# Kernel optimization log

Measured on AMD Instinct MI355X. Metric: run time of the kernel, lower is better.

Reference implementation:

```python
import jax, jax.numpy as jnp
import numpy as np

B, N, C, H, W = 256, 50000, 3, 32, 32


def setup_inputs() -> dict:
    key = jax.random.key(0)
    k1, k2, k3 = jax.random.split(key, 3)
    inp = jax.random.normal(k1, (B, C, H, W), dtype=jnp.float32)
    train_data = jax.random.normal(k2, (N, C, H, W), dtype=jnp.float32)
    # per-query noise levels in a realistic diffusion range
    sigma = jax.random.uniform(k3, (B,), dtype=jnp.float32) * 1.5 + 0.5
    return {"input": inp, "sigma": sigma, "train_data": train_data}


def reference(input, sigma, train_data):
    """Karras optimal denoiser:
    D(x, sigma) = sum_i y_i * Gau(x; y_i, sigma^2 I) / sum_i Gau(x; y_i, sigma^2 I).
    The Gaussian normalization constant (sigma*sqrt(2*pi))^D cancels in the ratio,
    so this is exactly softmax over -0.5*||x - y_i||^2 / sigma^2 (same math as the
    per-dim product of densities in the original, computed stably in log space).
    """
    b = input.shape[0]
    x = input.reshape(b, -1)                      # [B, D]
    y = train_data.reshape(train_data.shape[0], -1)  # [N, D]
    x2 = jnp.sum(x * x, axis=1, keepdims=True)    # [B, 1]
    y2 = jnp.sum(y * y, axis=1)                   # [N]
    # pairwise squared distances via GEMM: [B, N]
    sqdist = x2 + y2[None, :] - 2.0 * (x @ y.T)
    logw = -0.5 * sqdist / (sigma[:, None] ** 2)  # [B, N]
    w = jax.nn.softmax(logw, axis=1)              # normalized Gaussian weights
    out = w @ y                                   # [B, D] weighted average
    return out.reshape(input.shape)
```

## Files before the change

kernel.cpp:

```cpp
#include <hip/hip_runtime.h>
#include <hip/hip_bf16.h>
#include <type_traits>

#define BQ   256
#define NTR  50000
#define DD   3072
#define NSP  50048
#define NBLK 391
#define CAP  4096
#define DELTA 18.0f

typedef __fp16 f16;
typedef __fp16 f16x2 __attribute__((ext_vector_type(2)));
typedef __fp16 f16x8 __attribute__((ext_vector_type(8)));
typedef float  f32x4 __attribute__((ext_vector_type(4)));

__global__ __launch_bounds__(256) void kx(const float* __restrict__ x, f16* __restrict__ xp) {
    const int t = blockIdx.x * 256 + threadIdx.x;
    const int g = t >> 8, r = t & 255;
    const f32x4* src = (const f32x4*)(x + (size_t)r * DD + (g << 3));
    f32x4 a = src[0], b = src[1];
    union { f16x2 h2[4]; f16x8 h8; } u;
    u.h2[0] = __builtin_amdgcn_cvt_pkrtz(a[0], a[1]);
    u.h2[1] = __builtin_amdgcn_cvt_pkrtz(a[2], a[3]);
    u.h2[2] = __builtin_amdgcn_cvt_pkrtz(b[0], b[1]);
    u.h2[3] = __builtin_amdgcn_cvt_pkrtz(b[2], b[3]);
    ((f16x8*)xp)[t] = u.h8;
}

__global__ __launch_bounds__(256, 2) void kqk(
    const f16* __restrict__ xp, const float* __restrict__ y,
    float* __restrict__ S, float* __restrict__ pmax) {
    __shared__ char Bs[2][16384];

    const int tid = threadIdx.x;
    const int blk = blockIdx.x;
    const int n0  = blk * 128;

    const int ry   = tid >> 1;
    const int kp   = (tid & 1) << 5;
    const int yrow = n0 + ry;
    const bool yval = yrow < NTR;
    const float* ybase = y + (size_t)yrow * DD + kp;
    const int bsw = (ry & 7) << 4;
    int bo[4];
    #pragma unroll
    for (int j = 0; j < 4; ++j) bo[j] = ry * 128 + (((kp << 1) + (j << 4)) ^ bsw);

    const int w = tid >> 6, l = tid & 63;
    const int l15 = l & 15, lg = l >> 4;

    f32x4 acc[4][8] = {};
    float y2a = 0.f;
    f32x4 p[8];

    auto loady = [&](int ks) {
        if (yval) {
            const f32x4* pp = (const f32x4*)(ybase + (ks << 6));
            #pragma unroll
            for (int j = 0; j < 8; ++j) p[j] = pp[j];
        } else {
            #pragma unroll
            for (int j = 0; j < 8; ++j) p[j] = 0.f;
        }
    };
    auto cvtw = [&](int buf) {
        #pragma unroll
        for (int j = 0; j < 8; ++j)
            y2a += p[j][0]*p[j][0] + p[j][1]*p[j][1] + p[j][2]*p[j][2] + p[j][3]*p[j][3];
        union { f16x2 h2[4]; f16x8 h8; } u[4];
        #pragma unroll
        for (int j = 0; j < 4; ++j) {
            u[j].h2[0] = __builtin_amdgcn_cvt_pkrtz(p[2*j][0],   p[2*j][1]);
            u[j].h2[1] = __builtin_amdgcn_cvt_pkrtz(p[2*j][2],   p[2*j][3]);
            u[j].h2[2] = __builtin_amdgcn_cvt_pkrtz(p[2*j+1][0], p[2*j+1][1]);
            u[j].h2[3] = __builtin_amdgcn_cvt_pkrtz(p[2*j+1][2], p[2*j+1][3]);
            *(f16x8*)(&Bs[buf][bo[j]]) = u[j].h8;
        }
    };

    loady(0);
    cvtw(0);
    asm volatile("s_waitcnt lgkmcnt(0)" ::: "memory");
    __builtin_amdgcn_s_barrier();

    const f16x8* ap = (const f16x8*)xp;
    const int arow = (w << 6) + l15;

    for (int ks = 0; ks < 48; ++ks) {
        const int cur = ks & 1;
        if (ks + 1 < 48) loady(ks + 1);
        #pragma unroll
        for (int kk = 0; kk < 2; ++kk) {
            f16x8 af[4];
            #pragma unroll
            for (int fm = 0; fm < 4; ++fm)
                af[fm] = ap[(size_t)((ks << 3) + (kk << 2) + lg) * 256 + arow + (fm << 4)];
            #pragma unroll
            for (int fnh = 0; fnh < 2; ++fnh) {
                f16x8 bf[4];
                #pragma unroll
                for (int fj = 0; fj < 4; ++fj) {
                    int fn = (fnh << 2) + fj;
                    int r = (fn << 4) + l15;
                    bf[fj] = *(const f16x8*)(&Bs[cur][r * 128 + (((kk << 6) + (lg << 4)) ^ ((r & 7) << 4))]);
                }
                #pragma unroll
                for (int fm = 0; fm < 4; ++fm)
                    #pragma unroll
                    for (int fj = 0; fj < 4; ++fj)
                        acc[fm][(fnh << 2) + fj] =
                            __builtin_amdgcn_mfma_f32_16x16x32_f16(af[fm], bf[fj], acc[fm][(fnh << 2) + fj], 0, 0, 0);
            }
        }
        if (ks + 1 < 48) cvtw(cur ^ 1);
        asm volatile("s_waitcnt lgkmcnt(0)" ::: "memory");
        __builtin_amdgcn_s_barrier();
    }

    float* lys = (float*)&Bs[0][0];
    y2a += __shfl_xor(y2a, 1, 64);
    if ((tid & 1) == 0) lys[ry] = y2a;
    __syncthreads();
    float ly2[8];
    #pragma unroll
    for (int fn = 0; fn < 8; ++fn) ly2[fn] = 0.5f * lys[(fn << 4) + l15];
    #pragma unroll
    for (int fm = 0; fm < 4; ++fm) {
        #pragma unroll
        for (int j = 0; j < 4; ++j) {
            float rm = -3.4e38f;
            #pragma unroll
            for (int fn = 0; fn < 8; ++fn) {
                int col = n0 + (fn << 4) + l15;
                float sc = acc[fm][fn][j] - ly2[fn];
                rm = (col < NTR) ? fmaxf(rm, sc) : rm;
            }
            #pragma unroll
            for (int off = 1; off < 16; off <<= 1) rm = fmaxf(rm, __shfl_xor(rm, off, 64));
            if (l15 == 0)
                pmax[(size_t)((w << 6) + (fm << 4) + (lg << 2) + j) * NBLK + blk] = rm;
        }
    }
    #pragma unroll
    for (int fm = 0; fm < 4; ++fm) {
        int row0 = (w << 6) + (fm << 4) + (lg << 2);
        #pragma unroll
        for (int fn = 0; fn < 8; ++fn) {
            int col = n0 + (fn << 4) + l15;
            float* sp = S + (size_t)row0 * NSP + col;
            sp[0]               = acc[fm][fn][0] - ly2[fn];
            sp[NSP]             = acc[fm][fn][1] - ly2[fn];
            sp[2 * (size_t)NSP] = acc[fm][fn][2] - ly2[fn];
            sp[3 * (size_t)NSP] = acc[fm][fn][3] - ly2[fn];
        }
    }
}

__global__ __launch_bounds__(256) void ksel(
    const float* __restrict__ S, const float* __restrict__ pmax,
    const float* __restrict__ sig, unsigned* __restrict__ cnt,
    unsigned* __restrict__ cand) {
    __shared__ float red[4];
    const int b = blockIdx.x, tid = threadIdx.x;
    const float s2 = sig[b] * sig[b];
    const float* pm = pmax + (size_t)b * NBLK;
    float mx = -3.4e38f;
    for (int i = tid; i < NBLK; i += 256) mx = fmaxf(mx, pm[i]);
    #pragma unroll
    for (int o = 1; o < 64; o <<= 1) mx = fmaxf(mx, __shfl_xor(mx, o, 64));
    if ((tid & 63) == 0) red[tid >> 6] = mx;
    __syncthreads();
    mx = fmaxf(fmaxf(red[0], red[1]), fmaxf(red[2], red[3]));
    const float thr = mx - DELTA * s2;
    const f32x4* rowv = (const f32x4*)(S + (size_t)b * NSP);
    for (int i = tid; i < 12500; i += 256) {
        f32x4 s = rowv[i];
        #pragma unroll
        for (int j = 0; j < 4; ++j) {
            if (s[j] >= thr) {
                unsigned idx = atomicAdd(&cnt[b], 1u);
                if (idx < CAP) cand[(size_t)b * CAP + idx] = (unsigned)(4 * i + j);
            }
        }
    }
}

__global__ __launch_bounds__(512) void kpv(
    const float* __restrict__ x, const float* __restrict__ y,
    const float* __restrict__ sig, const unsigned* __restrict__ cnt,
    const unsigned* __restrict__ cand, float* __restrict__ out) {
    __shared__ float xs[DD];
    __shared__ unsigned ci[CAP];
    __shared__ float om[8], ol[8];
    __shared__ float sumv[DD];
    const int b = blockIdx.x, tid = threadIdx.x;
    const int c = (int)(cnt[b] < (unsigned)CAP ? cnt[b] : (unsigned)CAP);
    const float s2 = sig[b] * sig[b];
    const float isc = -0.5f / s2;
    for (int i = tid; i < DD; i += 512) xs[i] = x[(size_t)b * DD + i];
    for (int i = tid; i < c; i += 512) ci[i] = cand[(size_t)b * CAP + i];
    __syncthreads();
    const int w = tid >> 6, l = tid & 63;
    const f32x4* xr = (const f32x4*)xs;

    f32x4 o[12] = {};
    float m = -3.4e38f, ll = 0.f;
    f32x4 A[12], Bv[12];

    auto LD = [&](f32x4* dst, int i) {
        const f32x4* yr = (const f32x4*)(y + (size_t)ci[i] * DD);
        #pragma unroll
        for (int j = 0; j < 12; ++j) dst[j] = yr[(j << 6) + l];
    };
    auto PROC = [&](f32x4* src) {
        float d2 = 0.f;
        #pragma unroll
        for (int j = 0; j < 12; ++j) {
            f32x4 xv = xr[(j << 6) + l];
            float a0 = xv[0]-src[j][0], a1 = xv[1]-src[j][1],
                  a2 = xv[2]-src[j][2], a3 = xv[3]-src[j][3];
            d2 += a0*a0 + a1*a1 + a2*a2 + a3*a3;
        }
        #pragma unroll
        for (int off = 1; off < 64; off <<= 1) d2 += __shfl_xor(d2, off, 64);
        float s = d2 * isc;
        float mn = fmaxf(m, s);
        float f = __expf(m - mn);
        float wi = __expf(s - mn);
        #pragma unroll
        for (int j = 0; j < 12; ++j) o[j] = o[j] * f + wi * src[j];
        ll = ll * f + wi;
        m = mn;
    };

    int i = w;
    if (i < c) LD(A, i);
    for (; i < c; i += 16) {
        int i2 = i + 8;
        if (i2 < c) LD(Bv, i2);
        PROC(A);
        if (i2 < c) {
            if (i + 16 < c) LD(A, i + 16);
            PROC(Bv);
        }
    }
    om[w] = m; ol[w] = ll;
    __syncthreads();
    float M = om[0];
    #pragma unroll
    for (int ww = 1; ww < 8; ++ww) M = fmaxf(M, om[ww]);
    float Ls = 0.f;
    #pragma unroll
    for (int ww = 0; ww < 8; ++ww) Ls += ol[ww] * __expf(om[ww] - M);
    const float fw = __expf(m - M);
    f32x4* sv = (f32x4*)sumv;
    if (w == 0) {
        #pragma unroll
        for (int j = 0; j < 12; ++j) sv[(j << 6) + l] = o[j] * fw;
    }
    __syncthreads();
    for (int ww = 1; ww < 8; ++ww) {
        if (w == ww) {
            #pragma unroll
            for (int j = 0; j < 12; ++j) sv[(j << 6) + l] += o[j] * fw;
        }
        __syncthreads();
    }
    const float inv = 1.f / Ls;
    f32x4* od = (f32x4*)(out + (size_t)b * DD);
    for (int t = tid; t < 768; t += 512) od[t] = sv[t] * inv;
}

extern "C" void kernel_launch(void* const* d_in, const int* in_sizes, int n_in,
                              void* d_out, int out_size, void* d_ws, size_t ws_size,
                              hipStream_t stream) {
    const float* x   = (const float*)d_in[0];
    const float* sig = (const float*)d_in[1];
    const float* y   = (const float*)d_in[2];
    float* out = (float*)d_out;
    char* ws = (char*)d_ws;
    f16*      xp   = (f16*)(ws);
    unsigned* cnt  = (unsigned*)(ws + 1572864);
    unsigned* cand = (unsigned*)(ws + 1573888);
    float*    pmax = (float*)(ws + 5768192);
    float*    S    = (float*)(ws + 6568960);

    (void)hipMemsetAsync(cnt, 0, 256 * sizeof(unsigned), stream);
    kx  <<<384, 256, 0, stream>>>(x, xp);
    kqk <<<NBLK, 256, 0, stream>>>(xp, y, S, pmax);
    ksel<<<256, 256, 0, stream>>>(S, pmax, sig, cnt, cand);
    kpv <<<256, 512, 0, stream>>>(x, y, sig, cnt, cand, out);
}
```

Measured before the change: 303.3 us.

## Halve QK tile width to 64 columns, deepen K-step, add two-stage register prefetch

The score GEMM kernel now gives each block 64 training rows instead of 128, which doubles the block count to 782 so the GPU is better filled. The K-step per iteration grows from 64 to 128. A second register buffer prefetches the y tile two stages ahead, and the loop is unrolled in pairs so the shared-buffer index is a compile-time constant. The pmax layout and the workspace offset of S grow to match. In exchange, each block reuses the x fragments over fewer columns, so total x loads double, and holding more prefetch registers may reduce occupancy.

```diff
diff --git a/kernel.cpp b/kernel.cpp
--- a/kernel.cpp
+++ b/kernel.cpp
@@ -6,7 +6,7 @@
 #define NTR  50000
 #define DD   3072
 #define NSP  50048
-#define NBLK 391
+#define NBLK 782
 #define CAP  4096
 #define DELTA 18.0f
 
@@ -35,103 +35,107 @@
 
     const int tid = threadIdx.x;
     const int blk = blockIdx.x;
-    const int n0  = blk * 128;
-
-    const int ry   = tid >> 1;
-    const int kp   = (tid & 1) << 5;
+    const int n0  = blk * 64;
+
+    const int ry   = tid >> 2;
+    const int kp   = (tid & 3) << 5;
     const int yrow = n0 + ry;
     const bool yval = yrow < NTR;
     const float* ybase = y + (size_t)yrow * DD + kp;
     const int bsw = (ry & 7) << 4;
     int bo[4];
     #pragma unroll
-    for (int j = 0; j < 4; ++j) bo[j] = ry * 128 + (((kp << 1) + (j << 4)) ^ bsw);
+    for (int j = 0; j < 4; ++j) bo[j] = ry * 256 + ((((tid & 3) << 6) + (j << 4)) ^ bsw);
 
     const int w = tid >> 6, l = tid & 63;
     const int l15 = l & 15, lg = l >> 4;
 
-    f32x4 acc[4][8] = {};
+    f32x4 acc[4][4] = {};
     float y2a = 0.f;
-    f32x4 p[8];
-
-    auto loady = [&](int ks) {
+    f32x4 p[8], q[8];
+
+    auto loady = [&](f32x4* d, int ks) {
         if (yval) {
-            const f32x4* pp = (const f32x4*)(ybase + (ks << 6));
-            #pragma unroll
-            for (int j = 0; j < 8; ++j) p[j] = pp[j];
+            const f32x4* pp = (const f32x4*)(ybase + (ks << 7));
+            #pragma unroll
+            for (int j = 0; j < 8; ++j) d[j] = pp[j];
         } else {
             #pragma unroll
-            for (int j = 0; j < 8; ++j) p[j] = 0.f;
-        }
-    };
-    auto cvtw = [&](int buf) {
+            for (int j = 0; j < 8; ++j) d[j] = 0.f;
+        }
+    };
+    auto cvtw = [&](f32x4* d, int buf) {
         #pragma unroll
         for (int j = 0; j < 8; ++j)
-            y2a += p[j][0]*p[j][0] + p[j][1]*p[j][1] + p[j][2]*p[j][2] + p[j][3]*p[j][3];
+            y2a += d[j][0]*d[j][0] + d[j][1]*d[j][1] + d[j][2]*d[j][2] + d[j][3]*d[j][3];
         union { f16x2 h2[4]; f16x8 h8; } u[4];
         #pragma unroll
         for (int j = 0; j < 4; ++j) {
-            u[j].h2[0] = __builtin_amdgcn_cvt_pkrtz(p[2*j][0],   p[2*j][1]);
-            u[j].h2[1] = __builtin_amdgcn_cvt_pkrtz(p[2*j][2],   p[2*j][3]);
-            u[j].h2[2] = __builtin_amdgcn_cvt_pkrtz(p[2*j+1][0], p[2*j+1][1]);
-            u[j].h2[3] = __builtin_amdgcn_cvt_pkrtz(p[2*j+1][2], p[2*j+1][3]);
+            u[j].h2[0] = __builtin_amdgcn_cvt_pkrtz(d[2*j][0],   d[2*j][1]);
+            u[j].h2[1] = __builtin_amdgcn_cvt_pkrtz(d[2*j][2],   d[2*j][3]);
+            u[j].h2[2] = __builtin_amdgcn_cvt_pkrtz(d[2*j+1][0], d[2*j+1][1]);
+            u[j].h2[3] = __builtin_amdgcn_cvt_pkrtz(d[2*j+1][2], d[2*j+1][3]);
             *(f16x8*)(&Bs[buf][bo[j]]) = u[j].h8;
         }
     };
 
-    loady(0);
-    cvtw(0);
+    loady(p, 0);
+    loady(q, 1);
+    cvtw(p, 0);
     asm volatile("s_waitcnt lgkmcnt(0)" ::: "memory");
     __builtin_amdgcn_s_barrier();
 
     const f16x8* ap = (const f16x8*)xp;
     const int arow = (w << 6) + l15;
 
-    for (int ks = 0; ks < 48; ++ks) {
-        const int cur = ks & 1;
-        if (ks + 1 < 48) loady(ks + 1);
-        #pragma unroll
-        for (int kk = 0; kk < 2; ++kk) {
-            f16x8 af[4];
+    auto iter = [&](int ks, auto curC, f32x4* pre, f32x4* cvt) {
+        constexpr int cur = decltype(curC)::value;
+        f16x8 af[4][4];
+        #pragma unroll
+        for (int kk = 0; kk < 4; ++kk)
             #pragma unroll
             for (int fm = 0; fm < 4; ++fm)
-                af[fm] = ap[(size_t)((ks << 3) + (kk << 2) + lg) * 256 + arow + (fm << 4)];
-            #pragma unroll
-            for (int fnh = 0; fnh < 2; ++fnh) {
-                f16x8 bf[4];
+                af[kk][fm] = ap[(size_t)((ks << 4) + (kk << 2) + lg) * 256 + arow + (fm << 4)];
+        if (ks + 2 < 24) loady(pre, ks + 2);
+        #pragma unroll
+        for (int kk = 0; kk < 4; ++kk) {
+            f16x8 bf[4];
+            #pragma unroll
+            for (int fn = 0; fn < 4; ++fn) {
+                int r = (fn << 4) + l15;
+                bf[fn] = *(const f16x8*)(&Bs[cur][r * 256 + (((kk << 6) + (lg << 4)) ^ ((r & 7) << 4))]);
+            }
+            #pragma unroll
+            for (int fm = 0; fm < 4; ++fm)
                 #pragma unroll
-                for (int fj = 0; fj < 4; ++fj) {
-                    int fn = (fnh << 2) + fj;
-                    int r = (fn << 4) + l15;
-                    bf[fj] = *(const f16x8*)(&Bs[cur][r * 128 + (((kk << 6) + (lg << 4)) ^ ((r & 7) << 4))]);
-                }
-                #pragma unroll
-                for (int fm = 0; fm < 4; ++fm)
-                    #pragma unroll
-                    for (int fj = 0; fj < 4; ++fj)
-                        acc[fm][(fnh << 2) + fj] =
-                            __builtin_amdgcn_mfma_f32_16x16x32_f16(af[fm], bf[fj], acc[fm][(fnh << 2) + fj], 0, 0, 0);
-            }
-        }
-        if (ks + 1 < 48) cvtw(cur ^ 1);
+                for (int fn = 0; fn < 4; ++fn)
+                    acc[fm][fn] = __builtin_amdgcn_mfma_f32_16x16x32_f16(af[kk][fm], bf[fn], acc[fm][fn], 0, 0, 0);
+        }
+        if (ks + 1 < 24) cvtw(cvt, cur ^ 1);
         asm volatile("s_waitcnt lgkmcnt(0)" ::: "memory");
         __builtin_amdgcn_s_barrier();
+    };
+
+    for (int ks2 = 0; ks2 < 24; ks2 += 2) {
+        iter(ks2,     std::integral_constant<int,0>{}, p, q);
+        iter(ks2 + 1, std::integral_constant<int,1>{}, q, p);
     }
 
     float* lys = (float*)&Bs[0][0];
     y2a += __shfl_xor(y2a, 1, 64);
-    if ((tid & 1) == 0) lys[ry] = y2a;
-    __syncthreads();
-    float ly2[8];
-    #pragma unroll
-    for (int fn = 0; fn < 8; ++fn) ly2[fn] = 0.5f * lys[(fn << 4) + l15];
+    y2a += __shfl_xor(y2a, 2, 64);
+    if ((tid & 3) == 0) lys[ry] = y2a;
+    __syncthreads();
+    float ly2[4];
+    #pragma unroll
+    for (int fn = 0; fn < 4; ++fn) ly2[fn] = 0.5f * lys[(fn << 4) + l15];
     #pragma unroll
     for (int fm = 0; fm < 4; ++fm) {
         #pragma unroll
         for (int j = 0; j < 4; ++j) {
             float rm = -3.4e38f;
             #pragma unroll
-            for (int fn = 0; fn < 8; ++fn) {
+            for (int fn = 0; fn < 4; ++fn) {
                 int col = n0 + (fn << 4) + l15;
                 float sc = acc[fm][fn][j] - ly2[fn];
                 rm = (col < NTR) ? fmaxf(rm, sc) : rm;
@@ -146,7 +150,7 @@
     for (int fm = 0; fm < 4; ++fm) {
         int row0 = (w << 6) + (fm << 4) + (lg << 2);
         #pragma unroll
-        for (int fn = 0; fn < 8; ++fn) {
+        for (int fn = 0; fn < 4; ++fn) {
             int col = n0 + (fn << 4) + l15;
             float* sp = S + (size_t)row0 * NSP + col;
             sp[0]               = acc[fm][fn][0] - ly2[fn];
@@ -284,7 +288,7 @@
     unsigned* cnt  = (unsigned*)(ws + 1572864);
     unsigned* cand = (unsigned*)(ws + 1573888);
     float*    pmax = (float*)(ws + 5768192);
-    float*    S    = (float*)(ws + 6568960);
+    float*    S    = (float*)(ws + 8388608);
 
     (void)hipMemsetAsync(cnt, 0, 256 * sizeof(unsigned), stream);
     kx  <<<384, 256, 0, stream>>>(x, xp);
```

Result: no change. 304.6 us (+0.4%).
